# Kernel tuning notes

Measured on AMD Instinct MI355X. Metric: run time of the kernel, lower is better.

## Reference

```python
import jax, jax.numpy as jnp
import numpy as np

INPUT_DIM, HIDDEN, PROJ, OUT_DIM = 158, 128, 64, 22
B, T = 1024, 250
LN_EPS = 1e-5


def setup_inputs() -> dict:
    key = jax.random.key(0)
    ks = jax.random.split(key, 12)

    def xavier(k, shape):
        fan_out, fan_in = shape
        lim = np.sqrt(6.0 / (fan_in + fan_out))
        return jax.random.uniform(k, shape, jnp.float32, -lim, lim)

    def ortho(k, shape):
        a = jax.random.normal(k, shape, jnp.float32)
        q, r = jnp.linalg.qr(a)
        return q * jnp.sign(jnp.diag(r))[None, :]

    return {
        "x": jax.random.normal(ks[0], (B, T, INPUT_DIM), jnp.float32),
        "ln_gamma": jnp.ones((INPUT_DIM,), jnp.float32),
        "ln_beta": jnp.zeros((INPUT_DIM,), jnp.float32),
        # LSTM layer 0 (PyTorch gate order i,f,g,o stacked along dim 0)
        "W_ih0": xavier(ks[1], (4 * HIDDEN, INPUT_DIM)),
        "W_hh0": jnp.concatenate([ortho(jax.random.fold_in(ks[2], g), (HIDDEN, HIDDEN)) for g in range(4)], axis=0),
        "b0": jnp.zeros((4 * HIDDEN,), jnp.float32),
        # LSTM layer 1
        "W_ih1": xavier(ks[3], (4 * HIDDEN, HIDDEN)),
        "W_hh1": jnp.concatenate([ortho(jax.random.fold_in(ks[4], g), (HIDDEN, HIDDEN)) for g in range(4)], axis=0),
        "b1": jnp.zeros((4 * HIDDEN,), jnp.float32),
        # projection MLP
        "Wp1": xavier(ks[5], (PROJ, HIDDEN)),
        "bp1": jnp.zeros((PROJ,), jnp.float32),
        "Wp2": xavier(ks[6], (OUT_DIM, PROJ)),
        "bp2": jnp.zeros((OUT_DIM,), jnp.float32),
    }


def _lstm_layer(x, W_ih, W_hh, b):
    # x: [B, T, D] -> h_seq: [B, T, H]. Precompute input gates for all t.
    xg = jnp.einsum("btd,gd->btg", x, W_ih) + b           # [B, T, 4H]
    xg = jnp.swapaxes(xg, 0, 1)                            # [T, B, 4H]
    Bn = x.shape[0]
    h0 = jnp.zeros((Bn, HIDDEN), x.dtype)
    c0 = jnp.zeros((Bn, HIDDEN), x.dtype)

    def step(carry, xg_t):
        h, c = carry
        gates = xg_t + h @ W_hh.T                          # [B, 4H]
        i, f, g, o = jnp.split(gates, 4, axis=-1)
        i = jax.nn.sigmoid(i)
        f = jax.nn.sigmoid(f)
        g = jnp.tanh(g)
        o = jax.nn.sigmoid(o)
        c = f * c + i * g
        h = o * jnp.tanh(c)
        return (h, c), h

    _, h_seq = jax.lax.scan(step, (h0, c0), xg)            # [T, B, H]
    return jnp.swapaxes(h_seq, 0, 1)                       # [B, T, H]


def reference(x, ln_gamma, ln_beta, W_ih0, W_hh0, b0, W_ih1, W_hh1, b1, Wp1, bp1, Wp2, bp2):
    # LayerNorm over last dim
    mu = jnp.mean(x, axis=-1, keepdims=True)
    var = jnp.mean(jnp.square(x - mu), axis=-1, keepdims=True)
    xn = (x - mu) * jax.lax.rsqrt(var + LN_EPS) * ln_gamma + ln_beta
    # 2-layer LSTM
    h = _lstm_layer(xn, W_ih0, W_hh0, b0)
    h = _lstm_layer(h, W_ih1, W_hh1, b1)
    # projection MLP: Linear -> ReLU -> Linear
    p = jax.nn.relu(jnp.einsum("bth,ph->btp", h, Wp1) + bp1)
    return jnp.einsum("btp,op->bto", p, Wp2) + bp2
```

## Files before the change

kernel.cpp:

```cpp
#include <hip/hip_runtime.h>
#include <cstdint>

typedef _Float16 f16;
typedef _Float16 h8 __attribute__((ext_vector_type(8)));
typedef _Float16 h4 __attribute__((ext_vector_type(4)));
typedef float f4 __attribute__((ext_vector_type(4)));

#define NB 1024
#define NT 250
#define IND 158
#define KP0 160
#define NH 128
#define NG 512
#define LN_EPS 1e-5f

__device__ __forceinline__ float fast_sigmoid(float x) {
  float e = __builtin_amdgcn_exp2f(-1.44269504f * x);
  return __builtin_amdgcn_rcpf(1.f + e);
}
__device__ __forceinline__ float fast_tanh(float x) {
  float e = __builtin_amdgcn_exp2f(2.88539008f * x);
  return 1.f - 2.f * __builtin_amdgcn_rcpf(e + 1.f);
}

__global__ __launch_bounds__(256) void k_prep(const float* __restrict__ src, f16* __restrict__ dst,
                                              int srows, int scols, int dcols, int total) {
  int i = blockIdx.x * 256 + threadIdx.x;
  if (i >= total) return;
  int r = i / dcols, c = i - r * dcols;
  float v = (r < srows && c < scols) ? src[r * scols + c] : 0.f;
  dst[i] = (f16)v;
}

__global__ __launch_bounds__(256) void k_ln(const float* __restrict__ x, const float* __restrict__ gamma,
                                            const float* __restrict__ beta, f16* __restrict__ xn,
                                            int t0, int tc) {
  int tid = threadIdx.x;
  int sub = tid & 7;
  int rloc = tid >> 3;
  long long rowi = (long long)blockIdx.x * 32 + rloc;
  int b = (int)(rowi / tc), t = (int)(rowi % tc);
  const float* xr = x + ((long long)b * NT + (t0 + t)) * IND;
  float vals[20];
  float s = 0.f, ss = 0.f;
#pragma unroll
  for (int i = 0; i < 20; i++) {
    int k = sub + 8 * i;
    float v = (k < IND) ? xr[k] : 0.f;
    vals[i] = v; s += v; ss += v * v;
  }
  s += __shfl_xor(s, 1); ss += __shfl_xor(ss, 1);
  s += __shfl_xor(s, 2); ss += __shfl_xor(ss, 2);
  s += __shfl_xor(s, 4); ss += __shfl_xor(ss, 4);
  float mu = s * (1.f / IND);
  float var = ss * (1.f / IND) - mu * mu;
  float rs = rsqrtf(var + LN_EPS);
  f16* outr = xn + ((long long)b * tc + t) * KP0;
#pragma unroll
  for (int i = 0; i < 20; i++) {
    int k = sub + 8 * i;
    float v = (k < IND) ? (vals[i] - mu) * rs * gamma[k] + beta[k] : 0.f;
    outr[k] = (f16)v;
  }
}

template <int KP>
__global__ __launch_bounds__(256, 1) void k_gates(const f16* __restrict__ inp, long long tStride,
                                                  long long rowStride, const f16* __restrict__ W,
                                                  const float* __restrict__ bias, f16* __restrict__ xg) {
  constexpr int KPP = KP + 8;
  constexpr int KS = KP / 32;
  extern __shared__ f16 lds[];
  f16* Wl = lds;
  f16* Il = lds + 128 * KPP;
  int t = blockIdx.x, gs = blockIdx.y, bs = blockIdx.z;
  int tid = threadIdx.x;
  {
    int row = tid >> 1, half = tid & 1;
    const float4* srcw = (const float4*)(W + (gs * 128 + row) * KP) + half * (KP / 16);
    float4* dstw = (float4*)(Wl + row * KPP) + half * (KP / 16);
#pragma unroll
    for (int i = 0; i < KP / 16; i++) dstw[i] = srcw[i];
    const float4* srci = (const float4*)(inp + (long long)t * tStride + (long long)(bs * 128 + row) * rowStride) + half * (KP / 16);
    float4* dsti = (float4*)(Il + row * KPP) + half * (KP / 16);
#pragma unroll
    for (int i = 0; i < KP / 16; i++) dsti[i] = srci[i];
  }
  __syncthreads();
  int w = tid >> 6, lane = tid & 63, l15 = lane & 15, q = lane >> 4;
  h8 bf[2][KS];
#pragma unroll
  for (int nt = 0; nt < 2; nt++)
#pragma unroll
    for (int ks = 0; ks < KS; ks++)
      bf[nt][ks] = *(const h8*)(Il + (32 * w + 16 * nt + l15) * KPP + 32 * ks + 8 * q);
  f4 acc[8][2];
#pragma unroll
  for (int mt = 0; mt < 8; mt++) {
    float4 b4 = *(const float4*)(bias + gs * 128 + 16 * mt + 4 * q);
#pragma unroll
    for (int nt = 0; nt < 2; nt++) acc[mt][nt] = (f4){b4.x, b4.y, b4.z, b4.w};
  }
#pragma unroll
  for (int mt = 0; mt < 8; mt++) {
    h8 af[KS];
#pragma unroll
    for (int ks = 0; ks < KS; ks++)
      af[ks] = *(const h8*)(Wl + (16 * mt + l15) * KPP + 32 * ks + 8 * q);
#pragma unroll
    for (int nt = 0; nt < 2; nt++)
#pragma unroll
      for (int ks = 0; ks < KS; ks++)
        acc[mt][nt] = __builtin_amdgcn_mfma_f32_16x16x32_f16(af[ks], bf[nt][ks], acc[mt][nt], 0, 0, 0);
  }
#pragma unroll
  for (int mt = 0; mt < 8; mt++)
#pragma unroll
    for (int nt = 0; nt < 2; nt++) {
      h4 o4;
#pragma unroll
      for (int r = 0; r < 4; r++) o4[r] = (f16)acc[mt][nt][r];
      long long sample = bs * 128 + 32 * w + 16 * nt + l15;
      *(h4*)(xg + ((long long)t * NB + sample) * NG + gs * 128 + 16 * mt + 4 * q) = o4;
    }
}

__global__ __launch_bounds__(512, 2) void k_fused(const f16* __restrict__ xg, const f16* __restrict__ Whh0f,
                                                  const f16* __restrict__ Wih1f, const f16* __restrict__ Whh1f,
                                                  const float* __restrict__ b1, f16* __restrict__ hseq,
                                                  float* __restrict__ ch0, float* __restrict__ cc0,
                                                  float* __restrict__ ch1, float* __restrict__ cc1,
                                                  int tc, int first) {
  extern __shared__ f16 lds[];
  f16* WhhL = lds;
  f16* h0b = lds + 69632;
  f16* h1b = h0b + 4352;
  int tid = threadIdx.x;
  int w = tid >> 6, lane = tid & 63, l15 = lane & 15, q = lane >> 4;
  int b0 = blockIdx.x * 16;
  int jbase = 16 * w + 4 * q;

  {
    const unsigned long long* ws = (const unsigned long long*)Whh1f;
    unsigned long long* wd = (unsigned long long*)WhhL;
    for (int i = tid; i < 17408; i += 512) wd[i] = ws[i];
  }
  for (int i = tid; i < 2176; i += 512) {
    int n = i / 136, k = i - n * 136;
    float h0v = (!first && k < NH) ? ch0[(b0 + n) * NH + k] : 0.f;
    float h1v = (!first && k < NH) ? ch1[(b0 + n) * NH + k] : 0.f;
    h0b[i] = (f16)h0v;
    h0b[2176 + i] = (f16)0.f;
    h1b[i] = (f16)0.f;
    h1b[2176 + i] = (f16)h1v;
  }
  float c0r[4], c1r[4];
#pragma unroll
  for (int r = 0; r < 4; r++) {
    c0r[r] = first ? 0.f : cc0[(b0 + l15) * NH + jbase + r];
    c1r[r] = first ? 0.f : cc1[(b0 + l15) * NH + jbase + r];
  }
  h8 af0[4][4], af1[4][4];
#pragma unroll
  for (int g = 0; g < 4; g++)
#pragma unroll
    for (int ks = 0; ks < 4; ks++) {
      af0[g][ks] = *(const h8*)(Whh0f + (128 * g + 16 * w + l15) * 136 + 32 * ks + 8 * q);
      af1[g][ks] = *(const h8*)(Wih1f + (128 * g + 16 * w + l15) * 128 + 32 * ks + 8 * q);
    }
  f4 bias1[4];
#pragma unroll
  for (int g = 0; g < 4; g++) {
    float4 b4 = *(const float4*)(b1 + 128 * g + jbase);
    bias1[g] = (f4){b4.x, b4.y, b4.z, b4.w};
  }
  __syncthreads();

  const f16* xgb = xg + (long long)(b0 + l15) * NG + jbase;
  const long long tstep = (long long)NB * NG;
  h4 xa[4], xb[4], xc[4];
#pragma unroll
  for (int g = 0; g < 4; g++) xa[g] = *(const h4*)(xgb + 128 * g);
  if (tc > 1) {
#pragma unroll
    for (int g = 0; g < 4; g++) xb[g] = *(const h4*)(xgb + tstep + 128 * g);
  }
  h4 h0last, h1last;
  const int ldsrow = l15 * 136;

  for (int n = 0; n <= tc; n++) {
    int p = n & 1;
    h8 bf0[4];
#pragma unroll
    for (int ks = 0; ks < 4; ks++)
      bf0[ks] = *(const h8*)(h0b + p * 2176 + ldsrow + 32 * ks + 8 * q);
    if (n < tc) {
      f4 acc[4];
#pragma unroll
      for (int g = 0; g < 4; g++)
#pragma unroll
        for (int r = 0; r < 4; r++) acc[g][r] = (float)xa[g][r];
#pragma unroll
      for (int g = 0; g < 4; g++)
#pragma unroll
        for (int ks = 0; ks < 4; ks++)
          acc[g] = __builtin_amdgcn_mfma_f32_16x16x32_f16(af0[g][ks], bf0[ks], acc[g], 0, 0, 0);
      h4 hv;
#pragma unroll
      for (int r = 0; r < 4; r++) {
        float iv = fast_sigmoid(acc[0][r]);
        float fv = fast_sigmoid(acc[1][r]);
        float gv = fast_tanh(acc[2][r]);
        float ov = fast_sigmoid(acc[3][r]);
        float cc = fv * c0r[r] + iv * gv;
        c0r[r] = cc;
        hv[r] = (f16)(ov * fast_tanh(cc));
      }
      *(h4*)(h0b + (1 - p) * 2176 + ldsrow + jbase) = hv;
      h0last = hv;
    }
    if (n >= 1) {
      h8 bf1[4];
#pragma unroll
      for (int ks = 0; ks < 4; ks++)
        bf1[ks] = *(const h8*)(h1b + p * 2176 + ldsrow + 32 * ks + 8 * q);
      f4 acc[4];
#pragma unroll
      for (int g = 0; g < 4; g++) acc[g] = bias1[g];
#pragma unroll
      for (int g = 0; g < 4; g++)
#pragma unroll
        for (int ks = 0; ks < 4; ks++)
          acc[g] = __builtin_amdgcn_mfma_f32_16x16x32_f16(af1[g][ks], bf0[ks], acc[g], 0, 0, 0);
#pragma unroll
      for (int g = 0; g < 4; g++)
#pragma unroll
        for (int ks = 0; ks < 4; ks++) {
          h8 aw = *(const h8*)(WhhL + (128 * g + 16 * w + l15) * 136 + 32 * ks + 8 * q);
          acc[g] = __builtin_amdgcn_mfma_f32_16x16x32_f16(aw, bf1[ks], acc[g], 0, 0, 0);
        }
      h4 hv;
#pragma unroll
      for (int r = 0; r < 4; r++) {
        float iv = fast_sigmoid(acc[0][r]);
        float fv = fast_sigmoid(acc[1][r]);
        float gv = fast_tanh(acc[2][r]);
        float ov = fast_sigmoid(acc[3][r]);
        float cc = fv * c1r[r] + iv * gv;
        c1r[r] = cc;
        hv[r] = (f16)(ov * fast_tanh(cc));
      }
      *(h4*)(h1b + (1 - p) * 2176 + ldsrow + jbase) = hv;
      *(h4*)(hseq + ((long long)(n - 1) * NB + b0 + l15) * NH + jbase) = hv;
      h1last = hv;
    }
    if (n + 2 < tc) {
      const f16* xr = xgb + (long long)(n + 2) * tstep;
#pragma unroll
      for (int g = 0; g < 4; g++) xc[g] = *(const h4*)(xr + 128 * g);
    }
#pragma unroll
    for (int g = 0; g < 4; g++) { xa[g] = xb[g]; xb[g] = xc[g]; }
    asm volatile("s_waitcnt lgkmcnt(0)\n\ts_barrier" ::: "memory");
  }
#pragma unroll
  for (int r = 0; r < 4; r++) {
    int idx = (b0 + l15) * NH + jbase + r;
    cc0[idx] = c0r[r];
    cc1[idx] = c1r[r];
    ch0[idx] = (float)h0last[r];
    ch1[idx] = (float)h1last[r];
  }
}

__global__ __launch_bounds__(256, 1) void k_proj(const f16* __restrict__ hseq, const f16* __restrict__ Wp1f,
                                                 const f16* __restrict__ Wp2f, const float* __restrict__ bp1,
                                                 const float* __restrict__ bp2, float* __restrict__ out,
                                                 int tc, int t0) {
  extern __shared__ f16 lds[];
  f16* hl = lds;
  f16* w1 = hl + 128 * 136;
  f16* w2 = w1 + 64 * 136;
  f16* pl = w2 + 32 * 72;
  int t = blockIdx.x, bs = blockIdx.y;
  int tid = threadIdx.x;
  {
    int b = tid >> 1, half = tid & 1;
    const float4* s = (const float4*)(hseq + ((long long)t * NB + bs * 128 + b) * NH) + half * 8;
    float4* d = (float4*)(hl + b * 136) + half * 8;
#pragma unroll
    for (int i = 0; i < 8; i++) d[i] = s[i];
    if (tid < 128) {
      int row = tid >> 1;
      const float4* sw = (const float4*)(Wp1f + row * 128) + (tid & 1) * 8;
      float4* dw = (float4*)(w1 + row * 136) + (tid & 1) * 8;
#pragma unroll
      for (int i = 0; i < 8; i++) dw[i] = sw[i];
    } else if (tid < 192) {
      int t2 = tid - 128;
      int row = t2 >> 1;
      const float4* sw = (const float4*)(Wp2f + row * 64) + (t2 & 1) * 4;
      float4* dw = (float4*)(w2 + row * 72) + (t2 & 1) * 4;
#pragma unroll
      for (int i = 0; i < 4; i++) dw[i] = sw[i];
    }
  }
  __syncthreads();
  int w = tid >> 6, lane = tid & 63, l15 = lane & 15, q = lane >> 4;
  {
    h8 bf[4];
#pragma unroll
    for (int ks = 0; ks < 4; ks++)
      bf[ks] = *(const h8*)(w1 + (16 * w + l15) * 136 + 32 * ks + 8 * q);
    float bv = bp1[16 * w + l15];
#pragma unroll
    for (int mt = 0; mt < 8; mt++) {
      f4 acc = (f4){bv, bv, bv, bv};
#pragma unroll
      for (int ks = 0; ks < 4; ks++) {
        h8 a = *(const h8*)(hl + (16 * mt + l15) * 136 + 32 * ks + 8 * q);
        acc = __builtin_amdgcn_mfma_f32_16x16x32_f16(a, bf[ks], acc, 0, 0, 0);
      }
#pragma unroll
      for (int r = 0; r < 4; r++) {
        float v = acc[r] > 0.f ? acc[r] : 0.f;
        pl[(16 * mt + 4 * q + r) * 72 + 16 * w + l15] = (f16)v;
      }
    }
  }
  __syncthreads();
  {
    int nt = w & 1;
    int o = 16 * nt + l15;
    h8 bf2[2];
#pragma unroll
    for (int ks = 0; ks < 2; ks++)
      bf2[ks] = *(const h8*)(w2 + o * 72 + 32 * ks + 8 * q);
    float bv = (o < 22) ? bp2[o] : 0.f;
#pragma unroll
    for (int mi = 0; mi < 4; mi++) {
      int mt = (w >> 1) * 4 + mi;
      f4 acc = (f4){bv, bv, bv, bv};
#pragma unroll
      for (int ks = 0; ks < 2; ks++) {
        h8 a = *(const h8*)(pl + (16 * mt + l15) * 72 + 32 * ks + 8 * q);
        acc = __builtin_amdgcn_mfma_f32_16x16x32_f16(a, bf2[ks], acc, 0, 0, 0);
      }
      if (o < 22) {
#pragma unroll
        for (int r = 0; r < 4; r++) {
          int brow = bs * 128 + 16 * mt + 4 * q + r;
          out[((long long)brow * NT + (t0 + t)) * 22 + o] = acc[r];
        }
      }
    }
  }
}

extern "C" void kernel_launch(void* const* d_in, const int* in_sizes, int n_in,
                              void* d_out, int out_size, void* d_ws, size_t ws_size,
                              hipStream_t stream) {
  const float* x    = (const float*)d_in[0];
  const float* gam  = (const float*)d_in[1];
  const float* bet  = (const float*)d_in[2];
  const float* Wih0 = (const float*)d_in[3];
  const float* Whh0 = (const float*)d_in[4];
  const float* b0   = (const float*)d_in[5];
  const float* Wih1 = (const float*)d_in[6];
  const float* Whh1 = (const float*)d_in[7];
  const float* b1   = (const float*)d_in[8];
  const float* Wp1  = (const float*)d_in[9];
  const float* bp1  = (const float*)d_in[10];
  const float* Wp2  = (const float*)d_in[11];
  const float* bp2  = (const float*)d_in[12];
  float* out = (float*)d_out;

  uintptr_t base = (uintptr_t)d_ws;
  uintptr_t cur = base;
  auto alloc = [&](size_t bytes) { uintptr_t p = cur; cur += (bytes + 255) & ~(size_t)255; return (void*)p; };
  f16* Wih0f = (f16*)alloc((size_t)512 * 160 * 2);
  f16* Wih1f = (f16*)alloc((size_t)512 * 128 * 2);
  f16* Whh0f = (f16*)alloc((size_t)512 * 136 * 2);
  f16* Whh1f = (f16*)alloc((size_t)512 * 136 * 2);
  f16* Wp1f  = (f16*)alloc((size_t)64 * 128 * 2);
  f16* Wp2f  = (f16*)alloc((size_t)32 * 64 * 2);
  float* ch0 = (float*)alloc((size_t)1024 * 128 * 4);
  float* cc0 = (float*)alloc((size_t)1024 * 128 * 4);
  float* ch1 = (float*)alloc((size_t)1024 * 128 * 4);
  float* cc1 = (float*)alloc((size_t)1024 * 128 * 4);
  size_t fixed = cur - base;
  const size_t per_t = (size_t)1024 * 160 * 2 + (size_t)1024 * 512 * 2 + (size_t)1024 * 128 * 2;
  int tc = 1;
  const int cands[] = {250, 125, 50, 25, 10, 5, 2, 1};
  for (int cd : cands) {
    if (fixed + per_t * (size_t)cd + 4096 <= ws_size) { tc = cd; break; }
  }
  f16* xn  = (f16*)alloc((size_t)1024 * tc * 160 * 2);
  f16* xg  = (f16*)alloc((size_t)tc * 1024 * 512 * 2);
  f16* hsq = (f16*)alloc((size_t)tc * 1024 * 128 * 2);

  int lds1 = 2 * 128 * 168 * 2;
  int ldsF = (69632 + 4352 + 4352) * 2;
  int lds5 = (128 * 136 + 64 * 136 + 32 * 72 + 128 * 72) * 2;
  hipFuncSetAttribute(reinterpret_cast<const void*>(&k_gates<160>),
                      hipFuncAttributeMaxDynamicSharedMemorySize, lds1);
  hipFuncSetAttribute(reinterpret_cast<const void*>(&k_fused),
                      hipFuncAttributeMaxDynamicSharedMemorySize, ldsF);
  hipFuncSetAttribute(reinterpret_cast<const void*>(&k_proj),
                      hipFuncAttributeMaxDynamicSharedMemorySize, lds5);

  {
    struct Job { const float* s; f16* d; int sr, sc, dc, tot; };
    Job jobs[6] = {
        {Wih0, Wih0f, 512, 158, 160, 512 * 160},
        {Wih1, Wih1f, 512, 128, 128, 512 * 128},
        {Whh0, Whh0f, 512, 128, 136, 512 * 136},
        {Whh1, Whh1f, 512, 128, 136, 512 * 136},
        {Wp1,  Wp1f,  64, 128, 128, 64 * 128},
        {Wp2,  Wp2f,  22, 64, 64, 32 * 64},
    };
    for (int i = 0; i < 6; i++) {
      int g = (jobs[i].tot + 255) / 256;
      k_prep<<<g, 256, 0, stream>>>(jobs[i].s, jobs[i].d, jobs[i].sr, jobs[i].sc, jobs[i].dc, jobs[i].tot);
    }
  }

  int nch = NT / tc;
  for (int cidx = 0; cidx < nch; cidx++) {
    int t0 = cidx * tc;
    int first = (cidx == 0) ? 1 : 0;
    k_ln<<<dim3(1024 * tc / 32), 256, 0, stream>>>(x, gam, bet, xn, t0, tc);
    k_gates<160><<<dim3(tc, 4, 8), 256, lds1, stream>>>(xn, 160, (long long)tc * 160, Wih0f, b0, xg);
    k_fused<<<dim3(64), 512, ldsF, stream>>>(xg, Whh0f, Wih1f, Whh1f, b1, hsq, ch0, cc0, ch1, cc1, tc, first);
    k_proj<<<dim3(tc, 8), 256, lds5, stream>>>(hsq, Wp1f, Wp2f, bp1, bp2, out, tc, t0);
  }
}
```

Baseline: 1.052 ms.

## Hold all LSTM recurrent weights in registers with 4-wave fused blocks

The fused two-layer recurrence now runs 256 threads per block, and each wave handles two 16-row M tiles. All three weight matrices (Whh0, Wih1, Whh1) stay resident in registers, so Whh1 is no longer re-read from LDS every timestep. The xg layout written by k_gates is permuted so each lane can fetch its gate pre-activations with two contiguous 16-byte loads. Prefetch depth drops from two steps to one, and bias1 is stored in fp16. The cost is very high VGPR/AGPR pressure that could cause spills, plus half as many waves for the same per-step MFMA work, which serialises more MFMAs per wave.

```diff
diff --git a/kernel.cpp b/kernel.cpp
--- a/kernel.cpp
+++ b/kernel.cpp
@@ -121,156 +121,180 @@
 #pragma unroll
       for (int r = 0; r < 4; r++) o4[r] = (f16)acc[mt][nt][r];
       long long sample = bs * 128 + 32 * w + 16 * nt + l15;
-      *(h4*)(xg + ((long long)t * NB + sample) * NG + gs * 128 + 16 * mt + 4 * q) = o4;
-    }
-}
-
-__global__ __launch_bounds__(512, 2) void k_fused(const f16* __restrict__ xg, const f16* __restrict__ Whh0f,
+      *(h4*)(xg + ((long long)t * NB + sample) * NG + (4 * mt + q) * 16 + gs * 4) = o4;
+    }
+}
+
+__global__ __launch_bounds__(256, 1) void k_fused(const f16* __restrict__ xg, const f16* __restrict__ Whh0f,
                                                   const f16* __restrict__ Wih1f, const f16* __restrict__ Whh1f,
                                                   const float* __restrict__ b1, f16* __restrict__ hseq,
                                                   float* __restrict__ ch0, float* __restrict__ cc0,
                                                   float* __restrict__ ch1, float* __restrict__ cc1,
                                                   int tc, int first) {
-  extern __shared__ f16 lds[];
-  f16* WhhL = lds;
-  f16* h0b = lds + 69632;
-  f16* h1b = h0b + 4352;
+  __shared__ f16 h0b[2][16][136];
+  __shared__ f16 h1b[2][16][136];
   int tid = threadIdx.x;
   int w = tid >> 6, lane = tid & 63, l15 = lane & 15, q = lane >> 4;
   int b0 = blockIdx.x * 16;
-  int jbase = 16 * w + 4 * q;
-
-  {
-    const unsigned long long* ws = (const unsigned long long*)Whh1f;
-    unsigned long long* wd = (unsigned long long*)WhhL;
-    for (int i = tid; i < 17408; i += 512) wd[i] = ws[i];
-  }
-  for (int i = tid; i < 2176; i += 512) {
+
+  for (int i = tid; i < 2176; i += 256) {
     int n = i / 136, k = i - n * 136;
     float h0v = (!first && k < NH) ? ch0[(b0 + n) * NH + k] : 0.f;
     float h1v = (!first && k < NH) ? ch1[(b0 + n) * NH + k] : 0.f;
-    h0b[i] = (f16)h0v;
-    h0b[2176 + i] = (f16)0.f;
-    h1b[i] = (f16)0.f;
-    h1b[2176 + i] = (f16)h1v;
-  }
-  float c0r[4], c1r[4];
-#pragma unroll
-  for (int r = 0; r < 4; r++) {
-    c0r[r] = first ? 0.f : cc0[(b0 + l15) * NH + jbase + r];
-    c1r[r] = first ? 0.f : cc1[(b0 + l15) * NH + jbase + r];
-  }
-  h8 af0[4][4], af1[4][4];
-#pragma unroll
-  for (int g = 0; g < 4; g++)
-#pragma unroll
-    for (int ks = 0; ks < 4; ks++) {
-      af0[g][ks] = *(const h8*)(Whh0f + (128 * g + 16 * w + l15) * 136 + 32 * ks + 8 * q);
-      af1[g][ks] = *(const h8*)(Wih1f + (128 * g + 16 * w + l15) * 128 + 32 * ks + 8 * q);
-    }
-  f4 bias1[4];
-#pragma unroll
-  for (int g = 0; g < 4; g++) {
-    float4 b4 = *(const float4*)(b1 + 128 * g + jbase);
-    bias1[g] = (f4){b4.x, b4.y, b4.z, b4.w};
-  }
+    ((f16*)h0b)[i] = (f16)h0v;
+    ((f16*)h0b)[2176 + i] = (f16)0.f;
+    ((f16*)h1b)[i] = (f16)0.f;
+    ((f16*)h1b)[2176 + i] = (f16)h1v;
+  }
+  float c0r[2][4], c1r[2][4];
+#pragma unroll
+  for (int mt = 0; mt < 2; mt++)
+#pragma unroll
+    for (int r = 0; r < 4; r++) {
+      int u = 32 * w + 16 * mt + 4 * q + r;
+      c0r[mt][r] = first ? 0.f : cc0[(b0 + l15) * NH + u];
+      c1r[mt][r] = first ? 0.f : cc1[(b0 + l15) * NH + u];
+    }
+  h8 af0[2][4][4], af1[2][4][4], afhh[2][4][4];
+#pragma unroll
+  for (int mt = 0; mt < 2; mt++)
+#pragma unroll
+    for (int g = 0; g < 4; g++)
+#pragma unroll
+      for (int ks = 0; ks < 4; ks++) {
+        int row = 128 * g + 32 * w + 16 * mt + l15;
+        af0[mt][g][ks]  = *(const h8*)(Whh0f + row * 136 + 32 * ks + 8 * q);
+        af1[mt][g][ks]  = *(const h8*)(Wih1f + row * 128 + 32 * ks + 8 * q);
+        afhh[mt][g][ks] = *(const h8*)(Whh1f + row * 136 + 32 * ks + 8 * q);
+      }
+  h4 bias_h[2][4];
+#pragma unroll
+  for (int mt = 0; mt < 2; mt++)
+#pragma unroll
+    for (int g = 0; g < 4; g++) {
+      float4 b4 = *(const float4*)(b1 + 128 * g + 32 * w + 16 * mt + 4 * q);
+      bias_h[mt][g] = (h4){(f16)b4.x, (f16)b4.y, (f16)b4.z, (f16)b4.w};
+    }
   __syncthreads();
 
-  const f16* xgb = xg + (long long)(b0 + l15) * NG + jbase;
+  const f16* xgb = xg + (long long)(b0 + l15) * NG + (8 * w + q) * 16;
   const long long tstep = (long long)NB * NG;
-  h4 xa[4], xb[4], xc[4];
-#pragma unroll
-  for (int g = 0; g < 4; g++) xa[g] = *(const h4*)(xgb + 128 * g);
-  if (tc > 1) {
-#pragma unroll
-    for (int g = 0; g < 4; g++) xb[g] = *(const h4*)(xgb + tstep + 128 * g);
-  }
-  h4 h0last, h1last;
+  h8 xc0[2][2], xn0[2][2];
+#pragma unroll
+  for (int mt = 0; mt < 2; mt++) {
+    xc0[mt][0] = *(const h8*)(xgb + 64 * mt);
+    xc0[mt][1] = *(const h8*)(xgb + 64 * mt + 8);
+  }
+  h4 h0last[2], h1last[2];
   const int ldsrow = l15 * 136;
 
   for (int n = 0; n <= tc; n++) {
     int p = n & 1;
+    if (n + 1 < tc) {
+      const f16* xr = xgb + (long long)(n + 1) * tstep;
+#pragma unroll
+      for (int mt = 0; mt < 2; mt++) {
+        xn0[mt][0] = *(const h8*)(xr + 64 * mt);
+        xn0[mt][1] = *(const h8*)(xr + 64 * mt + 8);
+      }
+    }
     h8 bf0[4];
 #pragma unroll
     for (int ks = 0; ks < 4; ks++)
-      bf0[ks] = *(const h8*)(h0b + p * 2176 + ldsrow + 32 * ks + 8 * q);
+      bf0[ks] = *(const h8*)(&h0b[p][0][0] + ldsrow + 32 * ks + 8 * q);
     if (n < tc) {
-      f4 acc[4];
-#pragma unroll
-      for (int g = 0; g < 4; g++)
-#pragma unroll
-        for (int r = 0; r < 4; r++) acc[g][r] = (float)xa[g][r];
-#pragma unroll
-      for (int g = 0; g < 4; g++)
-#pragma unroll
-        for (int ks = 0; ks < 4; ks++)
-          acc[g] = __builtin_amdgcn_mfma_f32_16x16x32_f16(af0[g][ks], bf0[ks], acc[g], 0, 0, 0);
-      h4 hv;
-#pragma unroll
-      for (int r = 0; r < 4; r++) {
-        float iv = fast_sigmoid(acc[0][r]);
-        float fv = fast_sigmoid(acc[1][r]);
-        float gv = fast_tanh(acc[2][r]);
-        float ov = fast_sigmoid(acc[3][r]);
-        float cc = fv * c0r[r] + iv * gv;
-        c0r[r] = cc;
-        hv[r] = (f16)(ov * fast_tanh(cc));
-      }
-      *(h4*)(h0b + (1 - p) * 2176 + ldsrow + jbase) = hv;
-      h0last = hv;
+      f4 acc[2][4];
+#pragma unroll
+      for (int mt = 0; mt < 2; mt++)
+#pragma unroll
+        for (int g = 0; g < 4; g++)
+#pragma unroll
+          for (int r = 0; r < 4; r++) {
+            int idx = 4 * g + r;
+            acc[mt][g][r] = (float)((idx < 8) ? xc0[mt][0][idx] : xc0[mt][1][idx - 8]);
+          }
+#pragma unroll
+      for (int mt = 0; mt < 2; mt++)
+#pragma unroll
+        for (int g = 0; g < 4; g++)
+#pragma unroll
+          for (int ks = 0; ks < 4; ks++)
+            acc[mt][g] = __builtin_amdgcn_mfma_f32_16x16x32_f16(af0[mt][g][ks], bf0[ks], acc[mt][g], 0, 0, 0);
+#pragma unroll
+      for (int mt = 0; mt < 2; mt++) {
+        h4 hv;
+#pragma unroll
+        for (int r = 0; r < 4; r++) {
+          float iv = fast_sigmoid(acc[mt][0][r]);
+          float fv = fast_sigmoid(acc[mt][1][r]);
+          float gv = fast_tanh(acc[mt][2][r]);
+          float ov = fast_sigmoid(acc[mt][3][r]);
+          float cc = fv * c0r[mt][r] + iv * gv;
+          c0r[mt][r] = cc;
+          hv[r] = (f16)(ov * fast_tanh(cc));
+        }
+        *(h4*)(&h0b[1 - p][0][0] + ldsrow + 32 * w + 16 * mt + 4 * q) = hv;
+        h0last[mt] = hv;
+      }
     }
     if (n >= 1) {
       h8 bf1[4];
 #pragma unroll
       for (int ks = 0; ks < 4; ks++)
-        bf1[ks] = *(const h8*)(h1b + p * 2176 + ldsrow + 32 * ks + 8 * q);
-      f4 acc[4];
-#pragma unroll
-      for (int g = 0; g < 4; g++) acc[g] = bias1[g];
-#pragma unroll
-      for (int g = 0; g < 4; g++)
-#pragma unroll
-        for (int ks = 0; ks < 4; ks++)
-          acc[g] = __builtin_amdgcn_mfma_f32_16x16x32_f16(af1[g][ks], bf0[ks], acc[g], 0, 0, 0);
-#pragma unroll
-      for (int g = 0; g < 4; g++)
-#pragma unroll
-        for (int ks = 0; ks < 4; ks++) {
-          h8 aw = *(const h8*)(WhhL + (128 * g + 16 * w + l15) * 136 + 32 * ks + 8 * q);
-          acc[g] = __builtin_amdgcn_mfma_f32_16x16x32_f16(aw, bf1[ks], acc[g], 0, 0, 0);
+        bf1[ks] = *(const h8*)(&h1b[p][0][0] + ldsrow + 32 * ks + 8 * q);
+      f4 acc[2][4];
+#pragma unroll
+      for (int mt = 0; mt < 2; mt++)
+#pragma unroll
+        for (int g = 0; g < 4; g++)
+#pragma unroll
+          for (int r = 0; r < 4; r++) acc[mt][g][r] = (float)bias_h[mt][g][r];
+#pragma unroll
+      for (int mt = 0; mt < 2; mt++)
+#pragma unroll
+        for (int g = 0; g < 4; g++)
+#pragma unroll
+          for (int ks = 0; ks < 4; ks++)
+            acc[mt][g] = __builtin_amdgcn_mfma_f32_16x16x32_f16(af1[mt][g][ks], bf0[ks], acc[mt][g], 0, 0, 0);
+#pragma unroll
+      for (int mt = 0; mt < 2; mt++)
+#pragma unroll
+        for (int g = 0; g < 4; g++)
+#pragma unroll
+          for (int ks = 0; ks < 4; ks++)
+            acc[mt][g] = __builtin_amdgcn_mfma_f32_16x16x32_f16(afhh[mt][g][ks], bf1[ks], acc[mt][g], 0, 0, 0);
+#pragma unroll
+      for (int mt = 0; mt < 2; mt++) {
+        h4 hv;
+#pragma unroll
+        for (int r = 0; r < 4; r++) {
+          float iv = fast_sigmoid(acc[mt][0][r]);
+          float fv = fast_sigmoid(acc[mt][1][r]);
+          float gv = fast_tanh(acc[mt][2][r]);
+          float ov = fast_sigmoid(acc[mt][3][r]);
+          float cc = fv * c1r[mt][r] + iv * gv;
+          c1r[mt][r] = cc;
+          hv[r] = (f16)(ov * fast_tanh(cc));
         }
-      h4 hv;
-#pragma unroll
-      for (int r = 0; r < 4; r++) {
-        float iv = fast_sigmoid(acc[0][r]);
-        float fv = fast_sigmoid(acc[1][r]);
-        float gv = fast_tanh(acc[2][r]);
-        float ov = fast_sigmoid(acc[3][r]);
-        float cc = fv * c1r[r] + iv * gv;
-        c1r[r] = cc;
-        hv[r] = (f16)(ov * fast_tanh(cc));
-      }
-      *(h4*)(h1b + (1 - p) * 2176 + ldsrow + jbase) = hv;
-      *(h4*)(hseq + ((long long)(n - 1) * NB + b0 + l15) * NH + jbase) = hv;
-      h1last = hv;
-    }
-    if (n + 2 < tc) {
-      const f16* xr = xgb + (long long)(n + 2) * tstep;
-#pragma unroll
-      for (int g = 0; g < 4; g++) xc[g] = *(const h4*)(xr + 128 * g);
-    }
-#pragma unroll
-    for (int g = 0; g < 4; g++) { xa[g] = xb[g]; xb[g] = xc[g]; }
+        *(h4*)(&h1b[1 - p][0][0] + ldsrow + 32 * w + 16 * mt + 4 * q) = hv;
+        *(h4*)(hseq + ((long long)(n - 1) * NB + b0 + l15) * NH + 32 * w + 16 * mt + 4 * q) = hv;
+        h1last[mt] = hv;
+      }
+    }
+#pragma unroll
+    for (int mt = 0; mt < 2; mt++) { xc0[mt][0] = xn0[mt][0]; xc0[mt][1] = xn0[mt][1]; }
     asm volatile("s_waitcnt lgkmcnt(0)\n\ts_barrier" ::: "memory");
   }
 #pragma unroll
-  for (int r = 0; r < 4; r++) {
-    int idx = (b0 + l15) * NH + jbase + r;
-    cc0[idx] = c0r[r];
-    cc1[idx] = c1r[r];
-    ch0[idx] = (float)h0last[r];
-    ch1[idx] = (float)h1last[r];
-  }
+  for (int mt = 0; mt < 2; mt++)
+#pragma unroll
+    for (int r = 0; r < 4; r++) {
+      int idx = (b0 + l15) * NH + 32 * w + 16 * mt + 4 * q + r;
+      cc0[idx] = c0r[mt][r];
+      cc1[idx] = c1r[mt][r];
+      ch0[idx] = (float)h0last[mt][r];
+      ch1[idx] = (float)h1last[mt][r];
+    }
 }
 
 __global__ __launch_bounds__(256, 1) void k_proj(const f16* __restrict__ hseq, const f16* __restrict__ Wp1f,
@@ -400,12 +424,9 @@
   f16* hsq = (f16*)alloc((size_t)tc * 1024 * 128 * 2);
 
   int lds1 = 2 * 128 * 168 * 2;
-  int ldsF = (69632 + 4352 + 4352) * 2;
   int lds5 = (128 * 136 + 64 * 136 + 32 * 72 + 128 * 72) * 2;
   hipFuncSetAttribute(reinterpret_cast<const void*>(&k_gates<160>),
                       hipFuncAttributeMaxDynamicSharedMemorySize, lds1);
-  hipFuncSetAttribute(reinterpret_cast<const void*>(&k_fused),
-                      hipFuncAttributeMaxDynamicSharedMemorySize, ldsF);
   hipFuncSetAttribute(reinterpret_cast<const void*>(&k_proj),
                       hipFuncAttributeMaxDynamicSharedMemorySize, lds5);
 
@@ -431,7 +452,7 @@
     int first = (cidx == 0) ? 1 : 0;
     k_ln<<<dim3(1024 * tc / 32), 256, 0, stream>>>(x, gam, bet, xn, t0, tc);
     k_gates<160><<<dim3(tc, 4, 8), 256, lds1, stream>>>(xn, 160, (long long)tc * 160, Wih0f, b0, xg);
-    k_fused<<<dim3(64), 512, ldsF, stream>>>(xg, Whh0f, Wih1f, Whh1f, b1, hsq, ch0, cc0, ch1, cc1, tc, first);
+    k_fused<<<dim3(64), 256, 0, stream>>>(xg, Whh0f, Wih1f, Whh1f, b1, hsq, ch0, cc0, ch1, cc1, tc, first);
     k_proj<<<dim3(tc, 8), 256, lds5, stream>>>(hsq, Wp1f, Wp2f, bp1, bp2, out, tc, t0);
   }
 }
```

After: 1.490 ms. 1.42x slower.
